# Kernel optimization log

Hardware: AMD Instinct MI355X
Metric: run time of the kernel (lower is better)

Reference implementation:

```python
import jax, jax.numpy as jnp
import numpy as np
from jax import lax

DROP_PROB = 0.1
BLOCK_SIZE = 7
FEAT_SIZE = 56
GAMMA = DROP_PROB / BLOCK_SIZE ** 2 * (FEAT_SIZE ** 2 / (FEAT_SIZE - BLOCK_SIZE + 1) ** 2)


def setup_inputs() -> dict:
    key = jax.random.key(0)
    k1, k2 = jax.random.split(key)
    x = jax.random.normal(k1, (32, 256, 56, 56), dtype=jnp.float32)
    u = jax.random.uniform(k2, (56, 56), dtype=jnp.float32)
    return {"x": x, "u": u}


def reference(x, u):
    # Bernoulli(gamma) seed mask over (H, W)
    mask = (u < GAMMA).astype(x.dtype)
    # Original code scatters 1s at seed + offsets in [0, block)^2 (down/right),
    # then crops to (H, W). Equivalent: backward-looking max window of size block.
    dilated = lax.reduce_window(
        mask, jnp.array(0.0, x.dtype), lax.max,
        window_dimensions=(BLOCK_SIZE, BLOCK_SIZE),
        window_strides=(1, 1),
        padding=((BLOCK_SIZE - 1, 0), (BLOCK_SIZE - 1, 0)),
    )
    block_mask = 1.0 - dilated  # (H, W), 0 inside dropped blocks
    scale = block_mask.size / jnp.sum(block_mask)
    return x * block_mask[None, None, :, :] * scale
```

## Files before the change

kernel.cpp:

```cpp
#include <hip/hip_runtime.h>


#define HW    3136
#define WDIM  56
#define HDIM  56
#define HW4   784
#define ROWMASK 0x00FFFFFFFFFFFFFFull
#define NBLOCKS 2048
#define STRIDE  (NBLOCKS * 256u)
#define PSTEP   576u

typedef float vfloat4 __attribute__((ext_vector_type(4)));

__global__ void __launch_bounds__(256) dropblock_fused_kernel(
        const float* __restrict__ u, const vfloat4* __restrict__ x,
        vfloat4* __restrict__ out, unsigned int nvec) {
    __shared__ unsigned char seed[HW];
    __shared__ unsigned long long rowdil[HDIM];
    __shared__ unsigned long long dropbits[HDIM];
    __shared__ int rowkept[HDIM];
    __shared__ float s_scale;
    __shared__ vfloat4 m4s[HW4];

    const float gamma = (float)(0.1 / 49.0 * (3136.0 / 2500.0));

    for (int i = threadIdx.x; i < HW; i += 256)
        seed[i] = (u[i] < gamma) ? (unsigned char)1 : (unsigned char)0;
    __syncthreads();

    if (threadIdx.x < 64) {
        int r = threadIdx.x;
        if (r < HDIM) {
            unsigned long long rowmask = 0ull;
            const unsigned char* srow = &seed[r * WDIM];
            #pragma unroll
            for (int c = 0; c < WDIM; ++c)
                rowmask |= ((unsigned long long)srow[c]) << c;
            unsigned long long rd = rowmask;
            #pragma unroll
            for (int k = 1; k < 7; ++k) rd |= (rowmask << k);
            rd &= ROWMASK;
            rowdil[r] = rd;
        }
        __builtin_amdgcn_wave_barrier();
        if (r < HDIM) {
            int j0 = (r >= 6) ? r - 6 : 0;
            unsigned long long d = 0ull;
            for (int j = j0; j <= r; ++j) d |= rowdil[j];
            d &= ROWMASK;
            dropbits[r] = d;
            rowkept[r] = WDIM - __popcll(d);
        }
    }
    __syncthreads();

    if (threadIdx.x == 0) {
        int total = 0;
        for (int r = 0; r < HDIM; ++r) total += rowkept[r];
        s_scale = (float)HW / (float)total;
    }
    __syncthreads();

    {
        float scale = s_scale;
        float* mf = (float*)m4s;
        for (int i = threadIdx.x; i < HW; i += 256) {
            int r = i / WDIM, c = i % WDIM;
            mf[i] = ((dropbits[r] >> c) & 1ull) ? 0.0f : scale;
        }
    }
    __syncthreads();

    unsigned int i = blockIdx.x * 256u + threadIdx.x;
    unsigned int p = i % (unsigned int)HW4;
    for (; i < nvec; i += STRIDE) {
        vfloat4 xv = __builtin_nontemporal_load(&x[i]);
        vfloat4 o = xv * m4s[p];
        __builtin_nontemporal_store(o, &out[i]);
        p += PSTEP;
        if (p >= (unsigned int)HW4) p -= (unsigned int)HW4;
    }
}

extern "C" void kernel_launch(void* const* d_in, const int* in_sizes, int n_in,
                              void* d_out, int out_size, void* d_ws, size_t ws_size,
                              hipStream_t stream) {
    const float* x = (const float*)d_in[0];
    const float* u = (const float*)d_in[1];
    float* out = (float*)d_out;

    unsigned int nvec = (unsigned int)(out_size / 4);
    dropblock_fused_kernel<<<NBLOCKS, 256, 0, stream>>>(
        u, (const vfloat4*)x, (vfloat4*)out, nvec);
}
```

Baseline: 180.9 us.

## Keep per-thread mask in registers and overlap initial loads with mask construction

After: 185.8 us. +2.7%, slower.

```diff
diff --git a/kernel.cpp b/kernel.cpp
--- a/kernel.cpp
+++ b/kernel.cpp
@@ -1,84 +1,95 @@
 #include <hip/hip_runtime.h>
 
 
-#define HW    3136
-#define WDIM  56
-#define HDIM  56
-#define HW4   784
+#define HW      3136
+#define WDIM    56
+#define HDIM    56
+#define HW4     784
 #define ROWMASK 0x00FFFFFFFFFFFFFFull
-#define NBLOCKS 2048
+#define NBLOCKS 2009u
 #define STRIDE  (NBLOCKS * 256u)
-#define PSTEP   576u
 
 typedef float vfloat4 __attribute__((ext_vector_type(4)));
 
 __global__ void __launch_bounds__(256) dropblock_fused_kernel(
         const float* __restrict__ u, const vfloat4* __restrict__ x,
         vfloat4* __restrict__ out, unsigned int nvec) {
-    __shared__ unsigned char seed[HW];
-    __shared__ unsigned long long rowdil[HDIM];
+    __shared__ unsigned long long chunks[49];
     __shared__ unsigned long long dropbits[HDIM];
-    __shared__ int rowkept[HDIM];
     __shared__ float s_scale;
-    __shared__ vfloat4 m4s[HW4];
 
     const float gamma = (float)(0.1 / 49.0 * (3136.0 / 2500.0));
 
-    for (int i = threadIdx.x; i < HW; i += 256)
-        seed[i] = (u[i] < gamma) ? (unsigned char)1 : (unsigned char)0;
-    __syncthreads();
+    const unsigned int t = blockIdx.x * 256u + threadIdx.x;
 
-    if (threadIdx.x < 64) {
-        int r = threadIdx.x;
-        if (r < HDIM) {
-            unsigned long long rowmask = 0ull;
-            const unsigned char* srow = &seed[r * WDIM];
-            #pragma unroll
-            for (int c = 0; c < WDIM; ++c)
-                rowmask |= ((unsigned long long)srow[c]) << c;
-            unsigned long long rd = rowmask;
-            #pragma unroll
-            for (int k = 1; k < 7; ++k) rd |= (rowmask << k);
-            rd &= ROWMASK;
-            rowdil[r] = rd;
-        }
-        __builtin_amdgcn_wave_barrier();
-        if (r < HDIM) {
-            int j0 = (r >= 6) ? r - 6 : 0;
-            unsigned long long d = 0ull;
-            for (int j = j0; j <= r; ++j) d |= rowdil[j];
-            d &= ROWMASK;
-            dropbits[r] = d;
-            rowkept[r] = WDIM - __popcll(d);
-        }
+    vfloat4 a0 = x[t];
+    vfloat4 a1 = x[t + STRIDE];
+
+    const int lane = threadIdx.x & 63;
+    const int wave = threadIdx.x >> 6;
+
+    #pragma unroll
+    for (int k = 0; k < 12; ++k) {
+        unsigned long long b = __ballot(u[k * 256 + threadIdx.x] < gamma);
+        if (lane == 0) chunks[4 * k + wave] = b;
+    }
+    if (wave == 0) {
+        unsigned long long b = __ballot(u[3072 + lane] < gamma);
+        if (lane == 0) chunks[48] = b;
     }
     __syncthreads();
 
-    if (threadIdx.x == 0) {
-        int total = 0;
-        for (int r = 0; r < HDIM; ++r) total += rowkept[r];
-        s_scale = (float)HW / (float)total;
+    if (wave == 0) {
+        const int r = lane;
+        unsigned long long rd = 0ull;
+        if (r < HDIM) {
+            int bit = r * WDIM;
+            int a = bit >> 6, off = bit & 63;
+            unsigned long long row = chunks[a] >> off;
+            if (off > 8) row |= chunks[a + 1] << (64 - off);
+            row &= ROWMASK;
+            rd = row;
+            #pragma unroll
+            for (int k = 1; k < 7; ++k) rd |= row << k;
+            rd &= ROWMASK;
+        }
+        unsigned long long d = rd;
+        #pragma unroll
+        for (int k = 1; k <= 6; ++k)
+            d |= __shfl_up(rd, k);
+        int kept = 0;
+        if (r < HDIM) {
+            dropbits[r] = d;
+            kept = WDIM - __popcll(d);
+        }
+        #pragma unroll
+        for (int s = 32; s; s >>= 1) kept += __shfl_xor(kept, s);
+        if (lane == 0) s_scale = (float)HW / (float)kept;
     }
     __syncthreads();
 
     {
-        float scale = s_scale;
-        float* mf = (float*)m4s;
-        for (int i = threadIdx.x; i < HW; i += 256) {
-            int r = i / WDIM, c = i % WDIM;
-            mf[i] = ((dropbits[r] >> c) & 1ull) ? 0.0f : scale;
+        const unsigned int q = t % (unsigned int)HW4;
+        const int r = (int)q / 14;
+        const int c0 = ((int)q - r * 14) * 4;
+        const unsigned long long d = dropbits[r];
+        const float scale = s_scale;
+        vfloat4 m;
+        m[0] = ((d >> c0) & 1ull) ? 0.0f : scale;
+        m[1] = ((d >> (c0 + 1)) & 1ull) ? 0.0f : scale;
+        m[2] = ((d >> (c0 + 2)) & 1ull) ? 0.0f : scale;
+        m[3] = ((d >> (c0 + 3)) & 1ull) ? 0.0f : scale;
+
+        out[t] = a0 * m;
+        out[t + STRIDE] = a1 * m;
+        unsigned int i = t + 2u * STRIDE;
+        for (; i + STRIDE < nvec; i += 2u * STRIDE) {
+            vfloat4 b0 = x[i];
+            vfloat4 b1 = x[i + STRIDE];
+            out[i] = b0 * m;
+            out[i + STRIDE] = b1 * m;
         }
-    }
-    __syncthreads();
-
-    unsigned int i = blockIdx.x * 256u + threadIdx.x;
-    unsigned int p = i % (unsigned int)HW4;
-    for (; i < nvec; i += STRIDE) {
-        vfloat4 xv = __builtin_nontemporal_load(&x[i]);
-        vfloat4 o = xv * m4s[p];
-        __builtin_nontemporal_store(o, &out[i]);
-        p += PSTEP;
-        if (p >= (unsigned int)HW4) p -= (unsigned int)HW4;
+        if (i < nvec) out[i] = x[i] * m;
     }
 }
 
```
